# Kernel tuning notes

Measured on AMD Instinct MI355X. Metric: run time of the kernel, lower is better.

## Reference

```python
import jax, jax.numpy as jnp
from jax import lax
import numpy as np

B, C, H, W = 32, 3, 512, 512


def _erode3(m):
    # cv2.erode with 3x3 ones kernel == 3x3 min-pool; cv2's default border value
    # for erode is +inf, which matches reduce_window's min identity under SAME padding.
    return lax.reduce_window(m, jnp.inf, lax.min, (1, 3, 3), (1, 1, 1), 'SAME')


def _dilate3(m):
    # cv2.dilate with 3x3 ones kernel == 3x3 max-pool; default border -inf matches max identity.
    return lax.reduce_window(m, -jnp.inf, lax.max, (1, 3, 3), (1, 1, 1), 'SAME')


def setup_inputs() -> dict:
    key = jax.random.key(0)
    k1, k2 = jax.random.split(key)
    yhat = jax.random.normal(k1, (B, C, H, W), dtype=jnp.float32)
    y = jax.random.randint(k2, (B, H, W), 0, 3, dtype=jnp.int32)
    return {"yhat": yhat, "y": y}


def reference(yhat, y):
    # softmax + argmax over class dim (argmax(softmax(x)) == argmax(x), kept faithful)
    probas = jnp.argmax(jax.nn.softmax(yhat, axis=1), axis=1).astype(jnp.int32)  # [B,H,W]

    m1 = (y == 1).astype(jnp.float32)
    m2 = (y == 2).astype(jnp.float32)

    e1 = _erode3(m1)
    d1 = _dilate3(m1)
    e2 = _erode3(m2)
    d2 = _dilate3(m2)

    # class 2 assignment overrides class 1 (matches sequential masked assignment order)
    eroded = jnp.where(e2 == 1, 2, jnp.where(e1 == 1, 1, 0)).astype(jnp.int32)
    dilated = jnp.where(d2 == 1, 2, jnp.where(d1 == 1, 1, 0)).astype(jnp.int32)

    inter = jnp.logical_and(dilated == probas, dilated != 0)
    inter_count = jnp.sum(inter, axis=(1, 2))  # [B]
    uni = jnp.logical_or(eroded != 0, probas != 0)
    uni_count = jnp.sum(uni, axis=(1, 2))  # [B]

    score = inter_count.astype(jnp.float32) / uni_count.astype(jnp.float32)
    return jnp.mean(score)
```

## Files before the change

kernel.cpp:

```cpp
#include <hip/hip_runtime.h>

#define IMG_H 512
#define IMG_W 512
#define NB    32
#define HW    (IMG_H * IMG_W)
#define SEGS  32
#define RPB   8
#define GX    (IMG_H / RPB)
#define NPART GX

__global__ __launch_bounds__(256) void iou_kernel(const float* __restrict__ yhat,
                                                  const int* __restrict__ y,
                                                  unsigned long long* __restrict__ part) {
    const int b   = blockIdx.y;
    const int t   = blockIdx.x * 256 + threadIdx.x;
    const int h   = t >> 5;
    const int seg = t & 31;
    const int wbase = seg << 4;

    const int* yb = y + (size_t)b * HW;

    unsigned and1 = 0x3FFFFu, or1 = 0u, and2 = 0x3FFFFu, or2 = 0u;
    unsigned vmask = 0x3FFFFu;
    if (seg == 0)        vmask &= ~1u;
    if (seg == SEGS - 1) vmask &= ~(1u << 17);
    const unsigned inv = ~vmask;

    const int lane  = threadIdx.x & 63;
    const int laneL = (lane + 63) & 63;
    const int laneR = (lane + 1) & 63;

    #pragma unroll
    for (int dr = -1; dr <= 1; ++dr) {
        const int r = h + dr;
        const bool rv = (r >= 0) && (r < IMG_H);
        unsigned m1 = 0u, m2 = 0u;
        if (rv) {
            const int* row = yb + r * IMG_W + wbase;
            const int4 w0 = *reinterpret_cast<const int4*>(row);
            const int4 w1 = *reinterpret_cast<const int4*>(row + 4);
            const int4 w2 = *reinterpret_cast<const int4*>(row + 8);
            const int4 w3 = *reinterpret_cast<const int4*>(row + 12);
            const int c[16] = {w0.x, w0.y, w0.z, w0.w, w1.x, w1.y, w1.z, w1.w,
                               w2.x, w2.y, w2.z, w2.w, w3.x, w3.y, w3.z, w3.w};
            #pragma unroll
            for (int j = 0; j < 16; ++j) {
                m1 |= ((c[j] == 1) ? 1u : 0u) << j;
                m2 |= ((c[j] == 2) ? 1u : 0u) << j;
            }
        }
        const unsigned mm = m1 | (m2 << 16);
        const unsigned ml = __shfl(mm, laneL, 64);
        const unsigned mr = __shfl(mm, laneR, 64);
        if (rv) {
            const unsigned ext1 = (m1 << 1) | ((ml >> 15) & 1u) | ((mr & 1u) << 17);
            const unsigned ext2 = (m2 << 1) | (ml >> 31) | (((mr >> 16) & 1u) << 17);
            and1 &= (ext1 | inv);  or1 |= (ext1 & vmask);
            and2 &= (ext2 | inv);  or2 |= (ext2 & vmask);
        }
    }

    const unsigned E1 = and1 & (and1 >> 1) & (and1 >> 2);
    const unsigned E2 = and2 & (and2 >> 1) & (and2 >> 2);
    const unsigned D1 = or1  | (or1  >> 1) | (or1  >> 2);
    const unsigned D2 = or2  | (or2  >> 1) | (or2  >> 2);

    const float* yh = yhat + (size_t)b * 3 * HW + (size_t)h * IMG_W + wbase;
    float A[16], Bv[16], Cv[16];
    #pragma unroll
    for (int q = 0; q < 4; ++q) {
        const float4 va = *reinterpret_cast<const float4*>(yh + 4 * q);
        const float4 vb = *reinterpret_cast<const float4*>(yh + HW + 4 * q);
        const float4 vc = *reinterpret_cast<const float4*>(yh + 2 * HW + 4 * q);
        A[4*q+0]=va.x; A[4*q+1]=va.y; A[4*q+2]=va.z; A[4*q+3]=va.w;
        Bv[4*q+0]=vb.x; Bv[4*q+1]=vb.y; Bv[4*q+2]=vb.z; Bv[4*q+3]=vb.w;
        Cv[4*q+0]=vc.x; Cv[4*q+1]=vc.y; Cv[4*q+2]=vc.z; Cv[4*q+3]=vc.w;
    }
    unsigned P1 = 0u, P2 = 0u;
    #pragma unroll
    for (int j = 0; j < 16; ++j) {
        int   p    = 0;
        float best = A[j];
        if (Bv[j] > best) { best = Bv[j]; p = 1; }
        if (Cv[j] > best) {               p = 2; }
        P1 |= ((p == 1) ? 1u : 0u) << j;
        P2 |= ((p == 2) ? 1u : 0u) << j;
    }

    const unsigned inter = (unsigned)__popc((D2 & P2) | (D1 & ~D2 & P1));
    const unsigned uni   = (unsigned)__popc((E1 | E2 | P1 | P2) & 0xFFFFu);

    unsigned long long packed = (unsigned long long)inter | ((unsigned long long)uni << 32);
    #pragma unroll
    for (int off = 32; off > 0; off >>= 1)
        packed += __shfl_down(packed, off, 64);

    __shared__ unsigned long long wsum[4];
    const int wave = threadIdx.x >> 6;
    if ((threadIdx.x & 63) == 0) wsum[wave] = packed;
    __syncthreads();
    if (threadIdx.x == 0)
        part[(size_t)b * NPART + blockIdx.x] = wsum[0] + wsum[1] + wsum[2] + wsum[3];
}

__global__ void finalize_kernel(const unsigned long long* __restrict__ part,
                                float* __restrict__ out) {
    const int t = threadIdx.x;
    const int b = t >> 3;
    const int k = t & 7;
    unsigned long long s = 0ull;
    #pragma unroll
    for (int i = 0; i < 8; ++i)
        s += part[(size_t)b * NPART + k * 8 + i];
    s += __shfl_down(s, 4, 8);
    s += __shfl_down(s, 2, 8);
    s += __shfl_down(s, 1, 8);

    __shared__ float r[NB];
    if (k == 0) {
        const float inter = (float)(unsigned int)(s & 0xFFFFFFFFull);
        const float uni   = (float)(unsigned int)(s >> 32);
        r[b] = inter / uni;
    }
    __syncthreads();
    if (t < 32) {
        float v = r[t];
        #pragma unroll
        for (int off = 16; off > 0; off >>= 1)
            v += __shfl_down(v, off, 32);
        if (t == 0) out[0] = v / (float)NB;
    }
}

extern "C" void kernel_launch(void* const* d_in, const int* in_sizes, int n_in,
                              void* d_out, int out_size, void* d_ws, size_t ws_size,
                              hipStream_t stream) {
    const float* yhat = (const float*)d_in[0];
    const int*   y    = (const int*)d_in[1];
    float*       out  = (float*)d_out;
    unsigned long long* part = (unsigned long long*)d_ws;

    dim3 grid(GX, NB, 1);
    iou_kernel<<<grid, 256, 0, stream>>>(yhat, y, part);
    finalize_kernel<<<1, 256, 0, stream>>>(part, out);
}
```

Baseline: 29.73 us.

## Share label row masks via LDS instead of reloading three rows per thread

Each block now builds 64-bit class masks for 16 rows plus two halo rows once into shared memory. Threads read neighbour rows and segments from LDS instead of each thread reloading three label rows from global memory and shuffling edge bits. Each thread now covers 32 pixels rather than 16, which halves the grid and the partial count, so the finalize loop is adjusted. This cuts redundant label traffic by about 3x but adds a barrier, halo-load imbalance, and more registers per thread.

```diff
diff --git a/kernel.cpp b/kernel.cpp
--- a/kernel.cpp
+++ b/kernel.cpp
@@ -4,91 +4,126 @@
 #define IMG_W 512
 #define NB    32
 #define HW    (IMG_H * IMG_W)
-#define SEGS  32
-#define RPB   8
+#define SEGS  16
+#define RPB   16
 #define GX    (IMG_H / RPB)
 #define NPART GX
+
+struct MPair { unsigned long long m1, m2; };
+
+__device__ __forceinline__ MPair build_masks(const int* __restrict__ row) {
+    unsigned long long m1 = 0ull, m2 = 0ull;
+    #pragma unroll
+    for (int q = 0; q < 8; ++q) {
+        const int4 w = *reinterpret_cast<const int4*>(row + 4 * q);
+        m1 |= ((unsigned long long)(w.x == 1)) << (4 * q + 0);
+        m1 |= ((unsigned long long)(w.y == 1)) << (4 * q + 1);
+        m1 |= ((unsigned long long)(w.z == 1)) << (4 * q + 2);
+        m1 |= ((unsigned long long)(w.w == 1)) << (4 * q + 3);
+        m2 |= ((unsigned long long)(w.x == 2)) << (4 * q + 0);
+        m2 |= ((unsigned long long)(w.y == 2)) << (4 * q + 1);
+        m2 |= ((unsigned long long)(w.z == 2)) << (4 * q + 2);
+        m2 |= ((unsigned long long)(w.w == 2)) << (4 * q + 3);
+    }
+    MPair p; p.m1 = m1; p.m2 = m2; return p;
+}
 
 __global__ __launch_bounds__(256) void iou_kernel(const float* __restrict__ yhat,
                                                   const int* __restrict__ y,
                                                   unsigned long long* __restrict__ part) {
     const int b   = blockIdx.y;
-    const int t   = blockIdx.x * 256 + threadIdx.x;
-    const int h   = t >> 5;
-    const int seg = t & 31;
-    const int wbase = seg << 4;
+    const int rl  = threadIdx.x >> 4;
+    const int seg = threadIdx.x & 15;
+    const int h   = blockIdx.x * RPB + rl;
+    const int wb  = seg << 5;
 
     const int* yb = y + (size_t)b * HW;
 
-    unsigned and1 = 0x3FFFFu, or1 = 0u, and2 = 0x3FFFFu, or2 = 0u;
-    unsigned vmask = 0x3FFFFu;
-    if (seg == 0)        vmask &= ~1u;
-    if (seg == SEGS - 1) vmask &= ~(1u << 17);
-    const unsigned inv = ~vmask;
+    __shared__ MPair masks[RPB + 2][SEGS];
 
-    const int lane  = threadIdx.x & 63;
-    const int laneL = (lane + 63) & 63;
-    const int laneR = (lane + 1) & 63;
+    masks[rl + 1][seg] = build_masks(yb + (size_t)h * IMG_W + wb);
+    if (threadIdx.x < 2 * SEGS) {
+        const int s  = threadIdx.x;
+        const int hr = (s < SEGS) ? (blockIdx.x * RPB - 1) : (blockIdx.x * RPB + RPB);
+        const int sg = s & 15;
+        const int R  = (s < SEGS) ? 0 : (RPB + 1);
+        if ((unsigned)hr < IMG_H)
+            masks[R][sg] = build_masks(yb + (size_t)hr * IMG_W + (sg << 5));
+    }
+    __syncthreads();
+
+    unsigned long long andv1 = ~0ull, orv1 = 0ull, andv2 = ~0ull, orv2 = 0ull;
+    const int sL = (seg > 0) ? seg - 1 : 0;
+    const int sR = (seg < SEGS - 1) ? seg + 1 : SEGS - 1;
 
     #pragma unroll
     for (int dr = -1; dr <= 1; ++dr) {
-        const int r = h + dr;
-        const bool rv = (r >= 0) && (r < IMG_H);
-        unsigned m1 = 0u, m2 = 0u;
-        if (rv) {
-            const int* row = yb + r * IMG_W + wbase;
-            const int4 w0 = *reinterpret_cast<const int4*>(row);
-            const int4 w1 = *reinterpret_cast<const int4*>(row + 4);
-            const int4 w2 = *reinterpret_cast<const int4*>(row + 8);
-            const int4 w3 = *reinterpret_cast<const int4*>(row + 12);
-            const int c[16] = {w0.x, w0.y, w0.z, w0.w, w1.x, w1.y, w1.z, w1.w,
-                               w2.x, w2.y, w2.z, w2.w, w3.x, w3.y, w3.z, w3.w};
-            #pragma unroll
-            for (int j = 0; j < 16; ++j) {
-                m1 |= ((c[j] == 1) ? 1u : 0u) << j;
-                m2 |= ((c[j] == 2) ? 1u : 0u) << j;
-            }
-        }
-        const unsigned mm = m1 | (m2 << 16);
-        const unsigned ml = __shfl(mm, laneL, 64);
-        const unsigned mr = __shfl(mm, laneR, 64);
-        if (rv) {
-            const unsigned ext1 = (m1 << 1) | ((ml >> 15) & 1u) | ((mr & 1u) << 17);
-            const unsigned ext2 = (m2 << 1) | (ml >> 31) | (((mr >> 16) & 1u) << 17);
-            and1 &= (ext1 | inv);  or1 |= (ext1 & vmask);
-            and2 &= (ext2 | inv);  or2 |= (ext2 & vmask);
-        }
+        const int R = rl + 1 + dr;
+        const bool rv = (unsigned)(h + dr) < IMG_H;
+        const MPair mc = masks[R][seg];
+        const MPair mL = masks[R][sL];
+        const MPair mR = masks[R][sR];
+
+        const unsigned long long l1 = (mL.m1 >> 31) & 1ull;
+        const unsigned long long l2 = (mL.m2 >> 31) & 1ull;
+        const unsigned long long r1 = mR.m1 & 1ull;
+        const unsigned long long r2 = mR.m2 & 1ull;
+
+        const unsigned long long lA1 = (seg > 0) ? l1 : 1ull;
+        const unsigned long long lO1 = (seg > 0) ? l1 : 0ull;
+        const unsigned long long rA1 = (seg < SEGS - 1) ? r1 : 1ull;
+        const unsigned long long rO1 = (seg < SEGS - 1) ? r1 : 0ull;
+        const unsigned long long lA2 = (seg > 0) ? l2 : 1ull;
+        const unsigned long long lO2 = (seg > 0) ? l2 : 0ull;
+        const unsigned long long rA2 = (seg < SEGS - 1) ? r2 : 1ull;
+        const unsigned long long rO2 = (seg < SEGS - 1) ? r2 : 0ull;
+
+        const unsigned long long b1 = mc.m1 << 1;
+        const unsigned long long b2 = mc.m2 << 1;
+
+        andv1 &= rv ? (b1 | lA1 | (rA1 << 33)) : ~0ull;
+        orv1  |= rv ? (b1 | lO1 | (rO1 << 33)) : 0ull;
+        andv2 &= rv ? (b2 | lA2 | (rA2 << 33)) : ~0ull;
+        orv2  |= rv ? (b2 | lO2 | (rO2 << 33)) : 0ull;
     }
 
-    const unsigned E1 = and1 & (and1 >> 1) & (and1 >> 2);
-    const unsigned E2 = and2 & (and2 >> 1) & (and2 >> 2);
-    const unsigned D1 = or1  | (or1  >> 1) | (or1  >> 2);
-    const unsigned D2 = or2  | (or2  >> 1) | (or2  >> 2);
+    const unsigned long long E1 = andv1 & (andv1 >> 1) & (andv1 >> 2);
+    const unsigned long long E2 = andv2 & (andv2 >> 1) & (andv2 >> 2);
+    const unsigned long long D1 = orv1  | (orv1  >> 1) | (orv1  >> 2);
+    const unsigned long long D2 = orv2  | (orv2  >> 1) | (orv2  >> 2);
 
-    const float* yh = yhat + (size_t)b * 3 * HW + (size_t)h * IMG_W + wbase;
-    float A[16], Bv[16], Cv[16];
+    const float* yh = yhat + (size_t)b * 3 * HW + (size_t)h * IMG_W + wb;
+    unsigned long long P1 = 0ull, P2 = 0ull;
     #pragma unroll
-    for (int q = 0; q < 4; ++q) {
-        const float4 va = *reinterpret_cast<const float4*>(yh + 4 * q);
-        const float4 vb = *reinterpret_cast<const float4*>(yh + HW + 4 * q);
-        const float4 vc = *reinterpret_cast<const float4*>(yh + 2 * HW + 4 * q);
-        A[4*q+0]=va.x; A[4*q+1]=va.y; A[4*q+2]=va.z; A[4*q+3]=va.w;
-        Bv[4*q+0]=vb.x; Bv[4*q+1]=vb.y; Bv[4*q+2]=vb.z; Bv[4*q+3]=vb.w;
-        Cv[4*q+0]=vc.x; Cv[4*q+1]=vc.y; Cv[4*q+2]=vc.z; Cv[4*q+3]=vc.w;
-    }
-    unsigned P1 = 0u, P2 = 0u;
-    #pragma unroll
-    for (int j = 0; j < 16; ++j) {
-        int   p    = 0;
-        float best = A[j];
-        if (Bv[j] > best) { best = Bv[j]; p = 1; }
-        if (Cv[j] > best) {               p = 2; }
-        P1 |= ((p == 1) ? 1u : 0u) << j;
-        P2 |= ((p == 2) ? 1u : 0u) << j;
+    for (int half = 0; half < 2; ++half) {
+        const float* p0 = yh + 16 * half;
+        float A[16], Bv[16], Cv[16];
+        #pragma unroll
+        for (int q = 0; q < 4; ++q) {
+            const float4 va = *reinterpret_cast<const float4*>(p0 + 4 * q);
+            const float4 vb = *reinterpret_cast<const float4*>(p0 + HW + 4 * q);
+            const float4 vc = *reinterpret_cast<const float4*>(p0 + 2 * HW + 4 * q);
+            A[4*q+0]=va.x; A[4*q+1]=va.y; A[4*q+2]=va.z; A[4*q+3]=va.w;
+            Bv[4*q+0]=vb.x; Bv[4*q+1]=vb.y; Bv[4*q+2]=vb.z; Bv[4*q+3]=vb.w;
+            Cv[4*q+0]=vc.x; Cv[4*q+1]=vc.y; Cv[4*q+2]=vc.z; Cv[4*q+3]=vc.w;
+        }
+        unsigned p1 = 0u, p2 = 0u;
+        #pragma unroll
+        for (int j = 0; j < 16; ++j) {
+            int   p    = 0;
+            float best = A[j];
+            if (Bv[j] > best) { best = Bv[j]; p = 1; }
+            if (Cv[j] > best) {               p = 2; }
+            p1 |= ((p == 1) ? 1u : 0u) << j;
+            p2 |= ((p == 2) ? 1u : 0u) << j;
+        }
+        P1 |= ((unsigned long long)p1) << (16 * half);
+        P2 |= ((unsigned long long)p2) << (16 * half);
     }
 
-    const unsigned inter = (unsigned)__popc((D2 & P2) | (D1 & ~D2 & P1));
-    const unsigned uni   = (unsigned)__popc((E1 | E2 | P1 | P2) & 0xFFFFu);
+    const unsigned long long PIX = 0xFFFFFFFFull;
+    const unsigned inter = (unsigned)__popcll(((D2 & P2) | (D1 & ~D2 & P1)) & PIX);
+    const unsigned uni   = (unsigned)__popcll((E1 | E2 | P1 | P2) & PIX);
 
     unsigned long long packed = (unsigned long long)inter | ((unsigned long long)uni << 32);
     #pragma unroll
@@ -110,8 +145,8 @@
     const int k = t & 7;
     unsigned long long s = 0ull;
     #pragma unroll
-    for (int i = 0; i < 8; ++i)
-        s += part[(size_t)b * NPART + k * 8 + i];
+    for (int i = 0; i < 4; ++i)
+        s += part[(size_t)b * NPART + k * 4 + i];
     s += __shfl_down(s, 4, 8);
     s += __shfl_down(s, 2, 8);
     s += __shfl_down(s, 1, 8);
```

After: 34.72 us. 1.17x slower.

## Share label rows between wave halves via shuffle and hoist yhat loads

Applied to the files above, without the earlier changes.

Each wavefront covers two adjacent rows, so each half now loads its own row plus one outer neighbour row and gets the shared middle row from the partner half with a cross-half shuffle. This cuts per-thread label loads from three rows to two. The yhat float4 loads are also issued at kernel start so their latency overlaps the mask-building work. The cost is extra shuffles and live registers.

```diff
diff --git a/kernel.cpp b/kernel.cpp
--- a/kernel.cpp
+++ b/kernel.cpp
@@ -9,6 +9,23 @@
 #define GX    (IMG_H / RPB)
 #define NPART GX
 
+__device__ __forceinline__ unsigned build16(const int* __restrict__ row) {
+    unsigned m = 0u;
+    #pragma unroll
+    for (int q = 0; q < 4; ++q) {
+        const int4 w = *reinterpret_cast<const int4*>(row + 4 * q);
+        m |= ((w.x == 1) ? 1u : 0u) << (4 * q + 0);
+        m |= ((w.y == 1) ? 1u : 0u) << (4 * q + 1);
+        m |= ((w.z == 1) ? 1u : 0u) << (4 * q + 2);
+        m |= ((w.w == 1) ? 1u : 0u) << (4 * q + 3);
+        m |= ((w.x == 2) ? 1u : 0u) << (16 + 4 * q + 0);
+        m |= ((w.y == 2) ? 1u : 0u) << (16 + 4 * q + 1);
+        m |= ((w.z == 2) ? 1u : 0u) << (16 + 4 * q + 2);
+        m |= ((w.w == 2) ? 1u : 0u) << (16 + 4 * q + 3);
+    }
+    return m;
+}
+
 __global__ __launch_bounds__(256) void iou_kernel(const float* __restrict__ yhat,
                                                   const int* __restrict__ y,
                                                   unsigned long long* __restrict__ part) {
@@ -18,64 +35,73 @@
     const int seg = t & 31;
     const int wbase = seg << 4;
 
+    const int lane    = threadIdx.x & 63;
+    const bool lowHalf = (lane < 32);
+
+    const float* yh = yhat + (size_t)b * 3 * HW + (size_t)h * IMG_W + wbase;
+    float4 qa0 = *reinterpret_cast<const float4*>(yh);
+    float4 qa1 = *reinterpret_cast<const float4*>(yh + 4);
+    float4 qa2 = *reinterpret_cast<const float4*>(yh + 8);
+    float4 qa3 = *reinterpret_cast<const float4*>(yh + 12);
+    float4 qb0 = *reinterpret_cast<const float4*>(yh + HW);
+    float4 qb1 = *reinterpret_cast<const float4*>(yh + HW + 4);
+    float4 qb2 = *reinterpret_cast<const float4*>(yh + HW + 8);
+    float4 qb3 = *reinterpret_cast<const float4*>(yh + HW + 12);
+    float4 qc0 = *reinterpret_cast<const float4*>(yh + 2 * HW);
+    float4 qc1 = *reinterpret_cast<const float4*>(yh + 2 * HW + 4);
+    float4 qc2 = *reinterpret_cast<const float4*>(yh + 2 * HW + 8);
+    float4 qc3 = *reinterpret_cast<const float4*>(yh + 2 * HW + 12);
+
     const int* yb = y + (size_t)b * HW;
+    const int ho  = lowHalf ? (h - 1) : (h + 1);
+    const bool ov = (unsigned)ho < IMG_H;
+    const int hoc = ov ? ho : h;
 
-    unsigned and1 = 0x3FFFFu, or1 = 0u, and2 = 0x3FFFFu, or2 = 0u;
-    unsigned vmask = 0x3FFFFu;
+    const unsigned mOwn = build16(yb + (size_t)h   * IMG_W + wbase);
+    const unsigned mOut = build16(yb + (size_t)hoc * IMG_W + wbase);
+    const unsigned mPar = __shfl(mOwn, lane ^ 32, 64);
+
+    const unsigned mT = lowHalf ? mOut : mPar;
+    const unsigned mB = lowHalf ? mPar : mOut;
+    const bool vT = lowHalf ? ov : true;
+    const bool vB = lowHalf ? true : ov;
+
+    const int laneL = (lane + 63) & 63;
+    const int laneR = (lane + 1) & 63;
+    const unsigned tL = __shfl(mT, laneL, 64), tR = __shfl(mT, laneR, 64);
+    const unsigned cL = __shfl(mOwn, laneL, 64), cR = __shfl(mOwn, laneR, 64);
+    const unsigned bL = __shfl(mB, laneL, 64), bR = __shfl(mB, laneR, 64);
+
+    #define EXT1(m, ml, mr) ((((m) & 0xFFFFu) << 1) | (((ml) >> 15) & 1u) | (((mr) & 1u) << 17))
+    #define EXT2(m, ml, mr) ((((m) >> 16) << 1)     | ((ml) >> 31)        | ((((mr) >> 16) & 1u) << 17))
+    const unsigned eT1 = EXT1(mT, tL, tR),   eT2 = EXT2(mT, tL, tR);
+    const unsigned eC1 = EXT1(mOwn, cL, cR), eC2 = EXT2(mOwn, cL, cR);
+    const unsigned eB1 = EXT1(mB, bL, bR),   eB2 = EXT2(mB, bL, bR);
+
+    const unsigned ALL = 0x3FFFFu;
+    unsigned vmask = ALL;
     if (seg == 0)        vmask &= ~1u;
     if (seg == SEGS - 1) vmask &= ~(1u << 17);
-    const unsigned inv = ~vmask;
+    const unsigned inv = ALL & ~vmask;
 
-    const int lane  = threadIdx.x & 63;
-    const int laneL = (lane + 63) & 63;
-    const int laneR = (lane + 1) & 63;
-
-    #pragma unroll
-    for (int dr = -1; dr <= 1; ++dr) {
-        const int r = h + dr;
-        const bool rv = (r >= 0) && (r < IMG_H);
-        unsigned m1 = 0u, m2 = 0u;
-        if (rv) {
-            const int* row = yb + r * IMG_W + wbase;
-            const int4 w0 = *reinterpret_cast<const int4*>(row);
-            const int4 w1 = *reinterpret_cast<const int4*>(row + 4);
-            const int4 w2 = *reinterpret_cast<const int4*>(row + 8);
-            const int4 w3 = *reinterpret_cast<const int4*>(row + 12);
-            const int c[16] = {w0.x, w0.y, w0.z, w0.w, w1.x, w1.y, w1.z, w1.w,
-                               w2.x, w2.y, w2.z, w2.w, w3.x, w3.y, w3.z, w3.w};
-            #pragma unroll
-            for (int j = 0; j < 16; ++j) {
-                m1 |= ((c[j] == 1) ? 1u : 0u) << j;
-                m2 |= ((c[j] == 2) ? 1u : 0u) << j;
-            }
-        }
-        const unsigned mm = m1 | (m2 << 16);
-        const unsigned ml = __shfl(mm, laneL, 64);
-        const unsigned mr = __shfl(mm, laneR, 64);
-        if (rv) {
-            const unsigned ext1 = (m1 << 1) | ((ml >> 15) & 1u) | ((mr & 1u) << 17);
-            const unsigned ext2 = (m2 << 1) | (ml >> 31) | (((mr >> 16) & 1u) << 17);
-            and1 &= (ext1 | inv);  or1 |= (ext1 & vmask);
-            and2 &= (ext2 | inv);  or2 |= (ext2 & vmask);
-        }
-    }
+    unsigned and1 = eC1 & (vT ? eT1 : ALL) & (vB ? eB1 : ALL);
+    unsigned and2 = eC2 & (vT ? eT2 : ALL) & (vB ? eB2 : ALL);
+    unsigned or1  = eC1 | (vT ? eT1 : 0u)  | (vB ? eB1 : 0u);
+    unsigned or2  = eC2 | (vT ? eT2 : 0u)  | (vB ? eB2 : 0u);
+    and1 |= inv;  and2 |= inv;
+    or1  &= vmask; or2 &= vmask;
 
     const unsigned E1 = and1 & (and1 >> 1) & (and1 >> 2);
     const unsigned E2 = and2 & (and2 >> 1) & (and2 >> 2);
     const unsigned D1 = or1  | (or1  >> 1) | (or1  >> 2);
     const unsigned D2 = or2  | (or2  >> 1) | (or2  >> 2);
 
-    const float* yh = yhat + (size_t)b * 3 * HW + (size_t)h * IMG_W + wbase;
-    float A[16], Bv[16], Cv[16];
-    #pragma unroll
-    for (int q = 0; q < 4; ++q) {
-        const float4 va = *reinterpret_cast<const float4*>(yh + 4 * q);
-        const float4 vb = *reinterpret_cast<const float4*>(yh + HW + 4 * q);
-        const float4 vc = *reinterpret_cast<const float4*>(yh + 2 * HW + 4 * q);
-        A[4*q+0]=va.x; A[4*q+1]=va.y; A[4*q+2]=va.z; A[4*q+3]=va.w;
-        Bv[4*q+0]=vb.x; Bv[4*q+1]=vb.y; Bv[4*q+2]=vb.z; Bv[4*q+3]=vb.w;
-        Cv[4*q+0]=vc.x; Cv[4*q+1]=vc.y; Cv[4*q+2]=vc.z; Cv[4*q+3]=vc.w;
-    }
+    float A[16]  = {qa0.x,qa0.y,qa0.z,qa0.w, qa1.x,qa1.y,qa1.z,qa1.w,
+                    qa2.x,qa2.y,qa2.z,qa2.w, qa3.x,qa3.y,qa3.z,qa3.w};
+    float Bv[16] = {qb0.x,qb0.y,qb0.z,qb0.w, qb1.x,qb1.y,qb1.z,qb1.w,
+                    qb2.x,qb2.y,qb2.z,qb2.w, qb3.x,qb3.y,qb3.z,qb3.w};
+    float Cv[16] = {qc0.x,qc0.y,qc0.z,qc0.w, qc1.x,qc1.y,qc1.z,qc1.w,
+                    qc2.x,qc2.y,qc2.z,qc2.w, qc3.x,qc3.y,qc3.z,qc3.w};
     unsigned P1 = 0u, P2 = 0u;
     #pragma unroll
     for (int j = 0; j < 16; ++j) {
```

New measurement: 29.05 us. 2.3% less time.

## Stage label bitmasks in LDS with 2-row blocks and 4-pixel threads

Applied to the files above, without the earlier changes.

Each block now handles two image rows with 128 threads per row, each thread covering 4 pixels. Labels are packed into nibble masks and stored in shared memory along with one halo row, so neighbour pixels are read from LDS instead of cross-lane shuffles and three global row loads per thread. The aim is to cut redundant y reads (each row is read about twice instead of three times), give each thread less work and raise memory parallelism. The partial sums shrink to 16-bit-packed 32-bit words, which adds a barrier per block and quadruples the number of partials the finalize kernel has to sum. The packmask assumes labels are only 0,1,2.

```diff
diff --git a/kernel.cpp b/kernel.cpp
--- a/kernel.cpp
+++ b/kernel.cpp
@@ -4,81 +4,80 @@
 #define IMG_W 512
 #define NB    32
 #define HW    (IMG_H * IMG_W)
-#define SEGS  32
-#define RPB   8
-#define GX    (IMG_H / RPB)
-#define NPART GX
+#define NPART 256
+
+__device__ __forceinline__ unsigned packmask(const int4 w) {
+    const unsigned m1 = (unsigned)(w.x & 1)        | ((unsigned)(w.y & 1) << 1)
+                      | ((unsigned)(w.z & 1) << 2) | ((unsigned)(w.w & 1) << 3);
+    const unsigned m2 = (unsigned)(w.x >> 1)        | ((unsigned)(w.y >> 1) << 1)
+                      | ((unsigned)(w.z >> 1) << 2) | ((unsigned)(w.w >> 1) << 3);
+    return m1 | (m2 << 4);
+}
 
 __global__ __launch_bounds__(256) void iou_kernel(const float* __restrict__ yhat,
                                                   const int* __restrict__ y,
-                                                  unsigned long long* __restrict__ part) {
-    const int b   = blockIdx.y;
-    const int t   = blockIdx.x * 256 + threadIdx.x;
-    const int h   = t >> 5;
-    const int seg = t & 31;
-    const int wbase = seg << 4;
+                                                  unsigned* __restrict__ part) {
+    const int b    = blockIdx.y;
+    const int row0 = blockIdx.x << 1;
+    const int rs   = threadIdx.x >> 7;
+    const int c4   = threadIdx.x & 127;
+    const int h    = row0 + rs;
+
+    const float* yh = yhat + (size_t)b * 3 * HW + (size_t)h * IMG_W + (c4 << 2);
+    const float4 va = *reinterpret_cast<const float4*>(yh);
+    const float4 vb = *reinterpret_cast<const float4*>(yh + HW);
+    const float4 vc = *reinterpret_cast<const float4*>(yh + 2 * HW);
 
     const int* yb = y + (size_t)b * HW;
+    const int ho  = rs ? (h + 1) : (h - 1);
+    const int hoc = min(max(ho, 0), IMG_H - 1);
+    const int4 wOwn = *reinterpret_cast<const int4*>(yb + (size_t)h   * IMG_W + (c4 << 2));
+    const int4 wOut = *reinterpret_cast<const int4*>(yb + (size_t)hoc * IMG_W + (c4 << 2));
 
-    unsigned and1 = 0x3FFFFu, or1 = 0u, and2 = 0x3FFFFu, or2 = 0u;
-    unsigned vmask = 0x3FFFFu;
-    if (seg == 0)        vmask &= ~1u;
-    if (seg == SEGS - 1) vmask &= ~(1u << 17);
-    const unsigned inv = ~vmask;
+    __shared__ unsigned M[4][128];
+    M[rs + 1][c4]      = packmask(wOwn);
+    M[rs ? 3 : 0][c4]  = packmask(wOut);
+    __syncthreads();
 
-    const int lane  = threadIdx.x & 63;
-    const int laneL = (lane + 63) & 63;
-    const int laneR = (lane + 1) & 63;
+    const int cl = (c4 > 0)   ? c4 - 1 : 0;
+    const int cr = (c4 < 127) ? c4 + 1 : 127;
 
+    unsigned vmask = 0x3Fu;
+    if (c4 == 0)   vmask &= ~1u;
+    if (c4 == 127) vmask &= ~(1u << 5);
+    const unsigned inv = 0x3Fu & ~vmask;
+
+    unsigned and1 = 0x3Fu, or1 = 0u, and2 = 0x3Fu, or2 = 0u;
     #pragma unroll
-    for (int dr = -1; dr <= 1; ++dr) {
-        const int r = h + dr;
-        const bool rv = (r >= 0) && (r < IMG_H);
-        unsigned m1 = 0u, m2 = 0u;
-        if (rv) {
-            const int* row = yb + r * IMG_W + wbase;
-            const int4 w0 = *reinterpret_cast<const int4*>(row);
-            const int4 w1 = *reinterpret_cast<const int4*>(row + 4);
-            const int4 w2 = *reinterpret_cast<const int4*>(row + 8);
-            const int4 w3 = *reinterpret_cast<const int4*>(row + 12);
-            const int c[16] = {w0.x, w0.y, w0.z, w0.w, w1.x, w1.y, w1.z, w1.w,
-                               w2.x, w2.y, w2.z, w2.w, w3.x, w3.y, w3.z, w3.w};
-            #pragma unroll
-            for (int j = 0; j < 16; ++j) {
-                m1 |= ((c[j] == 1) ? 1u : 0u) << j;
-                m2 |= ((c[j] == 2) ? 1u : 0u) << j;
-            }
-        }
-        const unsigned mm = m1 | (m2 << 16);
-        const unsigned ml = __shfl(mm, laneL, 64);
-        const unsigned mr = __shfl(mm, laneR, 64);
-        if (rv) {
-            const unsigned ext1 = (m1 << 1) | ((ml >> 15) & 1u) | ((mr & 1u) << 17);
-            const unsigned ext2 = (m2 << 1) | (ml >> 31) | (((mr >> 16) & 1u) << 17);
-            and1 &= (ext1 | inv);  or1 |= (ext1 & vmask);
-            and2 &= (ext2 | inv);  or2 |= (ext2 & vmask);
-        }
+    for (int dr = 0; dr < 3; ++dr) {
+        const int s = rs + dr;
+        const bool valid = (s == 0) ? (row0 > 0)
+                         : (s == 3) ? (row0 + 2 < IMG_H)
+                         : true;
+        const unsigned L = M[s][cl];
+        const unsigned C = M[s][c4];
+        const unsigned R = M[s][cr];
+        const unsigned e1 = ((L >> 3) & 1u) | ((C & 0xFu) << 1) | ((R & 1u) << 5);
+        const unsigned e2 = ((L >> 7) & 1u) | (((C >> 4) & 0xFu) << 1) | (((R >> 4) & 1u) << 5);
+        and1 &= valid ? e1 : 0x3Fu;
+        and2 &= valid ? e2 : 0x3Fu;
+        or1  |= valid ? e1 : 0u;
+        or2  |= valid ? e2 : 0u;
     }
+    and1 |= inv;   and2 |= inv;
+    or1  &= vmask; or2  &= vmask;
 
     const unsigned E1 = and1 & (and1 >> 1) & (and1 >> 2);
     const unsigned E2 = and2 & (and2 >> 1) & (and2 >> 2);
     const unsigned D1 = or1  | (or1  >> 1) | (or1  >> 2);
     const unsigned D2 = or2  | (or2  >> 1) | (or2  >> 2);
 
-    const float* yh = yhat + (size_t)b * 3 * HW + (size_t)h * IMG_W + wbase;
-    float A[16], Bv[16], Cv[16];
-    #pragma unroll
-    for (int q = 0; q < 4; ++q) {
-        const float4 va = *reinterpret_cast<const float4*>(yh + 4 * q);
-        const float4 vb = *reinterpret_cast<const float4*>(yh + HW + 4 * q);
-        const float4 vc = *reinterpret_cast<const float4*>(yh + 2 * HW + 4 * q);
-        A[4*q+0]=va.x; A[4*q+1]=va.y; A[4*q+2]=va.z; A[4*q+3]=va.w;
-        Bv[4*q+0]=vb.x; Bv[4*q+1]=vb.y; Bv[4*q+2]=vb.z; Bv[4*q+3]=vb.w;
-        Cv[4*q+0]=vc.x; Cv[4*q+1]=vc.y; Cv[4*q+2]=vc.z; Cv[4*q+3]=vc.w;
-    }
+    const float A[4]  = {va.x, va.y, va.z, va.w};
+    const float Bv[4] = {vb.x, vb.y, vb.z, vb.w};
+    const float Cv[4] = {vc.x, vc.y, vc.z, vc.w};
     unsigned P1 = 0u, P2 = 0u;
     #pragma unroll
-    for (int j = 0; j < 16; ++j) {
+    for (int j = 0; j < 4; ++j) {
         int   p    = 0;
         float best = A[j];
         if (Bv[j] > best) { best = Bv[j]; p = 1; }
@@ -88,40 +87,40 @@
     }
 
     const unsigned inter = (unsigned)__popc((D2 & P2) | (D1 & ~D2 & P1));
-    const unsigned uni   = (unsigned)__popc((E1 | E2 | P1 | P2) & 0xFFFFu);
+    const unsigned uni   = (unsigned)__popc((E1 | E2 | P1 | P2) & 0xFu);
 
-    unsigned long long packed = (unsigned long long)inter | ((unsigned long long)uni << 32);
+    unsigned pk = inter | (uni << 16);
     #pragma unroll
     for (int off = 32; off > 0; off >>= 1)
-        packed += __shfl_down(packed, off, 64);
+        pk += __shfl_down(pk, off, 64);
 
-    __shared__ unsigned long long wsum[4];
+    __shared__ unsigned wsum[4];
     const int wave = threadIdx.x >> 6;
-    if ((threadIdx.x & 63) == 0) wsum[wave] = packed;
+    if ((threadIdx.x & 63) == 0) wsum[wave] = pk;
     __syncthreads();
     if (threadIdx.x == 0)
         part[(size_t)b * NPART + blockIdx.x] = wsum[0] + wsum[1] + wsum[2] + wsum[3];
 }
 
-__global__ void finalize_kernel(const unsigned long long* __restrict__ part,
+__global__ void finalize_kernel(const unsigned* __restrict__ part,
                                 float* __restrict__ out) {
     const int t = threadIdx.x;
     const int b = t >> 3;
     const int k = t & 7;
-    unsigned long long s = 0ull;
+    unsigned si = 0u, su = 0u;
     #pragma unroll
-    for (int i = 0; i < 8; ++i)
-        s += part[(size_t)b * NPART + k * 8 + i];
-    s += __shfl_down(s, 4, 8);
-    s += __shfl_down(s, 2, 8);
-    s += __shfl_down(s, 1, 8);
+    for (int i = 0; i < 32; ++i) {
+        const unsigned p = part[(size_t)b * NPART + k * 32 + i];
+        si += p & 0xFFFFu;
+        su += p >> 16;
+    }
+    si += __shfl_down(si, 4, 8);  su += __shfl_down(su, 4, 8);
+    si += __shfl_down(si, 2, 8);  su += __shfl_down(su, 2, 8);
+    si += __shfl_down(si, 1, 8);  su += __shfl_down(su, 1, 8);
 
     __shared__ float r[NB];
-    if (k == 0) {
-        const float inter = (float)(unsigned int)(s & 0xFFFFFFFFull);
-        const float uni   = (float)(unsigned int)(s >> 32);
-        r[b] = inter / uni;
-    }
+    if (k == 0)
+        r[b] = (float)si / (float)su;
     __syncthreads();
     if (t < 32) {
         float v = r[t];
@@ -138,9 +137,9 @@
     const float* yhat = (const float*)d_in[0];
     const int*   y    = (const int*)d_in[1];
     float*       out  = (float*)d_out;
-    unsigned long long* part = (unsigned long long*)d_ws;
+    unsigned*    part = (unsigned*)d_ws;
 
-    dim3 grid(GX, NB, 1);
+    dim3 grid(NPART, NB, 1);
     iou_kernel<<<grid, 256, 0, stream>>>(yhat, y, part);
     finalize_kernel<<<1, 256, 0, stream>>>(part, out);
 }
```

Measured after the change: 33.14 us. +11.5%, slower.
